# Optimization experiments

Hardware: AMD Instinct MI355X
Metric: run time of the kernel (lower is better)

Reference implementation:

```python
import jax, jax.numpy as jnp
import numpy as np

N = 50000      # nodes
E = 800000     # edges (avg degree 16)
DIN = 128      # input_dim
H = 256        # hidden_channels
DOUT = 64      # output_dim


def _glorot(k, shape):
    lim = float(np.sqrt(6.0 / (shape[0] + shape[1])))
    return jax.random.uniform(k, shape, jnp.float32, -lim, lim)


def setup_inputs() -> dict:
    key = jax.random.key(0)
    ks = jax.random.split(key, 10)
    return {
        "x": jax.random.normal(ks[0], (N, DIN), jnp.float32),
        "W1": _glorot(ks[3], (DIN, H)), "b1": jnp.zeros((H,), jnp.float32),
        "W2": _glorot(ks[4], (H, H)),   "b2": jnp.zeros((H,), jnp.float32),
        "L1w": _glorot(ks[5], (H, DIN)), "L1b": jnp.zeros((DIN,), jnp.float32),
        "L2w": _glorot(ks[6], (DIN, H)), "L2b": jnp.zeros((H,), jnp.float32),
        "W3": _glorot(ks[7], (H, DOUT)), "b3": jnp.zeros((DOUT,), jnp.float32),
        "adj": jax.random.randint(ks[1], (2, E), 0, N),
        "adj2": jax.random.randint(ks[2], (2, E), 0, N),
        "mode": 1,  # 1 -> 'l' (return logits); 0 -> softmax over classes
    }


def gcn_conv(x, edge_index, W, b):
    """PyG-style GCNConv: add self-loops, symmetric D^-1/2 A D^-1/2 norm,
    aggregate neighbor features, then (here fused) linear transform."""
    n = x.shape[0]
    loop = jnp.arange(n)
    src = jnp.concatenate([edge_index[0], loop])  # message sources (j)
    dst = jnp.concatenate([edge_index[1], loop])  # aggregation targets (i)
    deg = jax.ops.segment_sum(jnp.ones(src.shape[0], x.dtype), dst, num_segments=n)
    dinv = jax.lax.rsqrt(jnp.maximum(deg, 1.0))   # deg >= 1 due to self-loops
    norm = dinv[src] * dinv[dst]                  # [E+N]
    h = x @ W                                     # transform first (smaller of the two dims either way)
    msg = h[src] * norm[:, None]                  # gather + scale, [E+N, out]
    return jax.ops.segment_sum(msg, dst, num_segments=n) + b


def reference(x, W1, b1, W2, b2, L1w, L1b, L2w, L2b, W3, b3, adj, adj2, mode):
    h = jax.nn.relu(gcn_conv(x, adj, W1, b1))      # GCNConv(in->h) on adj
    h = jax.nn.relu(gcn_conv(h, adj2, W2, b2))     # GCNConv(h->h) on adj2
    h = jax.nn.relu(h @ L1w + L1b)                 # Linear(h->in)
    h = jax.nn.relu(h @ L2w + L2b)                 # Linear(in->h)
    out = gcn_conv(h, adj2, W3, b3)                # GCNConv(h->out) on adj2
    # dropout has p=0 -> identity
    return out if mode == 1 else jax.nn.softmax(out, axis=1)
```

## Files before the change

### kernel.cpp

```cpp
#include <hip/hip_runtime.h>
#include <hip/hip_bf16.h>
#include <cstdint>
#include <cstddef>

#define NNODES 50000
#define NEDGES 800000
#define D_IN   128
#define D_H    256
#define D_OUT  64
#define BSH    9
#define BKN    (1 << BSH)
#define NBKT   ((NNODES + BKN - 1) / BKN)
#define MAXB   12288
#define CHUNK  2048
#define QMAX   32639.0f

typedef __attribute__((ext_vector_type(8))) short bf16x8;
typedef __attribute__((ext_vector_type(4))) float f32x4;
typedef __attribute__((ext_vector_type(4))) int   i32x4;

__device__ __forceinline__ unsigned short f2bf(float f) {
    unsigned u = __builtin_bit_cast(unsigned, f);
    unsigned r = (u + 0x7FFFu + ((u >> 16) & 1u)) >> 16;
    return (unsigned short)r;
}
__device__ __forceinline__ float bf2f(unsigned short h) {
    unsigned u = ((unsigned)h) << 16;
    return __builtin_bit_cast(float, u);
}


__global__ __launch_bounds__(256) void k_bin(const int* __restrict__ adjA, const int* __restrict__ adjB,
                                             int* __restrict__ bcnt, unsigned* __restrict__ binned, int e) {
    __shared__ int h[NBKT], pfx[NBKT], put[NBKT], gbase[NBKT];
    __shared__ unsigned stage[CHUNK];
    const int g = blockIdx.y;
    const int* srcp = g ? adjB : adjA;
    const int* dstp = srcp + e;
    unsigned* outp = binned + (size_t)g * NBKT * MAXB;
    int* bc = bcnt + g * NBKT;
    const int tid = threadIdx.x;
    const int base = blockIdx.x * CHUNK;
    const int nrem = min(CHUNK, e - base);
    if (nrem <= 0) return;

    for (int t = tid; t < NBKT; t += 256) { h[t] = 0; put[t] = 0; }
    __syncthreads();

    unsigned pv[8];
    int bv[8];
    #pragma unroll
    for (int q = 0; q < 8; ++q) {
        int i = base + q * 256 + tid;
        bv[q] = -1;
        if (i < e) {
            int s = srcp[i];
            int d = dstp[i];
            pv[q] = ((unsigned)d << 16) | (unsigned)s;
            bv[q] = d >> BSH;
            atomicAdd(&h[bv[q]], 1);
        }
    }
    __syncthreads();
    if (tid == 0) {
        int r = 0;
        for (int k = 0; k < NBKT; ++k) { pfx[k] = r; r += h[k]; }
    }
    __syncthreads();
    #pragma unroll
    for (int q = 0; q < 8; ++q) {
        if (bv[q] >= 0) {
            int p = pfx[bv[q]] + atomicAdd(&put[bv[q]], 1);
            stage[p] = pv[q];
        }
    }
    __syncthreads();
    if (tid < NBKT && h[tid] > 0) gbase[tid] = atomicAdd(&bc[tid], h[tid]);
    __syncthreads();
    for (int idx = tid; idx < nrem; idx += 256) {
        unsigned v = stage[idx];
        int bb = v >> (16 + BSH);
        outp[(size_t)bb * MAXB + gbase[bb] + (idx - pfx[bb])] = v;
    }
}

__global__ void k_bktscan(const int* __restrict__ bcnt, int* __restrict__ bbase,
                          int* __restrict__ rp1, int* __restrict__ rp2) {
    __shared__ int s[2][NBKT];
    int t = threadIdx.x;
    if (t < NBKT) s[0][t] = bcnt[t];
    else if (t < 2 * NBKT) s[1][t - NBKT] = bcnt[t];
    __syncthreads();
    if (t < 2) {
        int r = 0;
        for (int k = 0; k < NBKT; ++k) { int v = s[t][k]; s[t][k] = r; r += v; }
    }
    __syncthreads();
    if (t < NBKT) bbase[t] = s[0][t];
    else if (t < 2 * NBKT) bbase[t] = s[1][t - NBKT];
    if (t == 0) { rp1[NNODES] = NEDGES; rp2[NNODES] = NEDGES; }
}

__global__ __launch_bounds__(256) void k_csr_bucket(const unsigned* __restrict__ binned,
                                                    const int* __restrict__ bcnt, const int* __restrict__ bbase,
                                                    int* __restrict__ rp1, int* __restrict__ rp2,
                                                    float* __restrict__ dinv1, float* __restrict__ dinv2,
                                                    int* __restrict__ col1, int* __restrict__ col2, int n) {
    __shared__ int lc[BKN];
    __shared__ int loff[BKN];
    __shared__ int ps[256];
    __shared__ int srt[MAXB];
    const int g = blockIdx.y;
    const int b = blockIdx.x;
    const unsigned* in = binned + (size_t)g * NBKT * MAXB + (size_t)b * MAXB;
    int* rp = g ? rp2 : rp1;
    float* dinv = g ? dinv2 : dinv1;
    int* col = g ? col2 : col1;
    const int nb = bcnt[g * NBKT + b];
    const int base0 = bbase[g * NBKT + b];
    const int nodebase = b << BSH;
    const int tid = threadIdx.x;

    for (int t = tid; t < BKN; t += 256) lc[t] = 0;
    __syncthreads();
    for (int t = tid; t < nb; t += 256)
        atomicAdd(&lc[(in[t] >> 16) & (BKN - 1)], 1);
    __syncthreads();
    int c0 = lc[2 * tid], c1 = lc[2 * tid + 1];
    int pair = c0 + c1;
    int sum = pair;
    ps[tid] = pair;
    __syncthreads();
    #pragma unroll
    for (int off = 1; off < 256; off <<= 1) {
        int u = (tid >= off) ? ps[tid - off] : 0;
        __syncthreads();
        sum += u;
        ps[tid] = sum;
        __syncthreads();
    }
    int excl = sum - pair;
    loff[2 * tid] = excl;
    loff[2 * tid + 1] = excl + c0;
    __syncthreads();
    for (int t = tid; t < BKN; t += 256) {
        int node = nodebase + t;
        if (node < n) {
            rp[node] = base0 + loff[t];
            dinv[node] = rsqrtf((float)(lc[t] + 1));
        }
    }
    __syncthreads();
    for (int t = tid; t < nb; t += 256) {
        unsigned v = in[t];
        int pos = atomicAdd(&loff[(v >> 16) & (BKN - 1)], 1);
        srt[pos] = (int)(v & 0xFFFFu);
    }
    __syncthreads();
    for (int t = tid; t < nb; t += 256) col[base0 + t] = srt[t];
}


template<int F, bool PRESCALE>
__global__ __launch_bounds__(256) void k_quant(const float* __restrict__ in, const float* __restrict__ dscale,
                                               short* __restrict__ q, float* __restrict__ qs, int n) {
    constexpr int VPT = F / 64;
    const int lane = threadIdx.x & 63;
    const int i = blockIdx.x * 4 + (threadIdx.x >> 6);
    if (i >= n) return;
    float v[VPT];
    const float* p = in + (size_t)i * F + lane * VPT;
    if constexpr (VPT == 4) { float4 t = *(const float4*)p; v[0] = t.x; v[1] = t.y; v[2] = t.z; v[3] = t.w; }
    else if constexpr (VPT == 2) { float2 t = *(const float2*)p; v[0] = t.x; v[1] = t.y; }
    else v[0] = *p;
    if constexpr (PRESCALE) {
        float d = dscale[i];
        #pragma unroll
        for (int c = 0; c < VPT; ++c) v[c] *= d;
    }
    float m = 0.f;
    #pragma unroll
    for (int c = 0; c < VPT; ++c) m = fmaxf(m, fabsf(v[c]));
    #pragma unroll
    for (int off = 32; off > 0; off >>= 1) m = fmaxf(m, __shfl_xor(m, off));
    float inv = (m > 0.f) ? 32767.0f / m : 0.f;
    short* qp = q + (size_t)i * F + lane * VPT;
    if constexpr (VPT == 4) {
        short4 o;
        o.x = (short)__float2int_rn(v[0] * inv);
        o.y = (short)__float2int_rn(v[1] * inv);
        o.z = (short)__float2int_rn(v[2] * inv);
        o.w = (short)__float2int_rn(v[3] * inv);
        *(short4*)qp = o;
    } else if constexpr (VPT == 2) {
        short2 o;
        o.x = (short)__float2int_rn(v[0] * inv);
        o.y = (short)__float2int_rn(v[1] * inv);
        *(short2*)qp = o;
    } else {
        *qp = (short)__float2int_rn(v[0] * inv);
    }
    if (lane == 0) qs[i] = m * (1.0f / 32767.0f);
}


template<int F, int OUTM>
__global__ __launch_bounds__(256) void k_agg3(const short* __restrict__ q, const float* __restrict__ qs,
                                              const int* __restrict__ rp, const int* __restrict__ col,
                                              const float* __restrict__ dinv, const float* __restrict__ bias,
                                              void* __restrict__ outv, float* __restrict__ qs_out, int n) {
    constexpr int VPT = F / 64;
    const int lane = threadIdx.x & 63;
    const int i = blockIdx.x * 4 + (threadIdx.x >> 6);
    if (i >= n) return;
    const short* ql = q + lane * VPT;
    float acc[VPT];
    #pragma unroll
    for (int c = 0; c < VPT; ++c) acc[c] = 0.f;

    int k = rp[i], end = rp[i + 1];

    auto body1 = [&](int j) {
        float s = qs[j];
        const short* pj = ql + (size_t)j * F;
        if constexpr (VPT == 4) {
            short4 v = *(const short4*)pj;
            acc[0] += s * (float)v.x; acc[1] += s * (float)v.y;
            acc[2] += s * (float)v.z; acc[3] += s * (float)v.w;
        } else if constexpr (VPT == 2) {
            short2 v = *(const short2*)pj;
            acc[0] += s * (float)v.x; acc[1] += s * (float)v.y;
        } else {
            acc[0] += s * (float)(*pj);
        }
    };

    body1(i);
    if constexpr (VPT == 4) {
        for (; k + 8 <= end; k += 8) {
            int j[8]; float s[8]; short4 v[8];
            #pragma unroll
            for (int u = 0; u < 8; ++u) j[u] = col[k + u];
            #pragma unroll
            for (int u = 0; u < 8; ++u) s[u] = qs[j[u]];
            #pragma unroll
            for (int u = 0; u < 8; ++u) v[u] = *(const short4*)(ql + (size_t)j[u] * F);
            #pragma unroll
            for (int u = 0; u < 8; ++u) {
                acc[0] += s[u] * (float)v[u].x; acc[1] += s[u] * (float)v[u].y;
                acc[2] += s[u] * (float)v[u].z; acc[3] += s[u] * (float)v[u].w;
            }
        }
    } else if constexpr (VPT == 2) {
        for (; k + 8 <= end; k += 8) {
            int j[8]; float s[8]; short2 v[8];
            #pragma unroll
            for (int u = 0; u < 8; ++u) j[u] = col[k + u];
            #pragma unroll
            for (int u = 0; u < 8; ++u) s[u] = qs[j[u]];
            #pragma unroll
            for (int u = 0; u < 8; ++u) v[u] = *(const short2*)(ql + (size_t)j[u] * F);
            #pragma unroll
            for (int u = 0; u < 8; ++u) {
                acc[0] += s[u] * (float)v[u].x; acc[1] += s[u] * (float)v[u].y;
            }
        }
    }
    for (; k + 4 <= end; k += 4) {
        int j0 = col[k], j1 = col[k + 1], j2 = col[k + 2], j3 = col[k + 3];
        float s0 = qs[j0], s1 = qs[j1], s2 = qs[j2], s3 = qs[j3];
        if constexpr (VPT == 4) {
            short4 v0 = *(const short4*)(ql + (size_t)j0 * F);
            short4 v1 = *(const short4*)(ql + (size_t)j1 * F);
            short4 v2 = *(const short4*)(ql + (size_t)j2 * F);
            short4 v3 = *(const short4*)(ql + (size_t)j3 * F);
            acc[0] += s0 * (float)v0.x + s1 * (float)v1.x + s2 * (float)v2.x + s3 * (float)v3.x;
            acc[1] += s0 * (float)v0.y + s1 * (float)v1.y + s2 * (float)v2.y + s3 * (float)v3.y;
            acc[2] += s0 * (float)v0.z + s1 * (float)v1.z + s2 * (float)v2.z + s3 * (float)v3.z;
            acc[3] += s0 * (float)v0.w + s1 * (float)v1.w + s2 * (float)v2.w + s3 * (float)v3.w;
        } else if constexpr (VPT == 2) {
            short2 v0 = *(const short2*)(ql + (size_t)j0 * F);
            short2 v1 = *(const short2*)(ql + (size_t)j1 * F);
            short2 v2 = *(const short2*)(ql + (size_t)j2 * F);
            short2 v3 = *(const short2*)(ql + (size_t)j3 * F);
            acc[0] += s0 * (float)v0.x + s1 * (float)v1.x + s2 * (float)v2.x + s3 * (float)v3.x;
            acc[1] += s0 * (float)v0.y + s1 * (float)v1.y + s2 * (float)v2.y + s3 * (float)v3.y;
        } else {
            float v0 = (float)ql[(size_t)j0 * F];
            float v1 = (float)ql[(size_t)j1 * F];
            float v2 = (float)ql[(size_t)j2 * F];
            float v3 = (float)ql[(size_t)j3 * F];
            acc[0] += s0 * v0 + s1 * v1 + s2 * v2 + s3 * v3;
        }
    }
    for (; k < end; ++k) body1(col[k]);

    float di = dinv[i];
    if constexpr (OUTM == 0) {
        float vals[VPT];
        float m = 0.f;
        #pragma unroll
        for (int c = 0; c < VPT; ++c) { vals[c] = acc[c] * di; m = fmaxf(m, fabsf(vals[c])); }
        #pragma unroll
        for (int off = 32; off > 0; off >>= 1) m = fmaxf(m, __shfl_xor(m, off));
        float inv = (m > 0.f) ? QMAX / m : 0.f;
        unsigned ph = 0, pl = 0;
        #pragma unroll
        for (int c = 0; c < VPT; ++c) {
            int qv = __float2int_rn(vals[c] * inv);
            int ah = (qv + 128) >> 8;
            int al = qv - (ah << 8);
            ph |= (unsigned)(ah & 0xFF) << (8 * c);
            pl |= (unsigned)(al & 0xFF) << (8 * c);
        }
        unsigned char* o8h = (unsigned char*)outv;
        unsigned char* o8l = o8h + (size_t)n * F;
        if constexpr (VPT == 4) {
            *(unsigned*)(o8h + (size_t)i * F + lane * 4) = ph;
            *(unsigned*)(o8l + (size_t)i * F + lane * 4) = pl;
        } else if constexpr (VPT == 2) {
            *(unsigned short*)(o8h + (size_t)i * F + lane * 2) = (unsigned short)ph;
            *(unsigned short*)(o8l + (size_t)i * F + lane * 2) = (unsigned short)pl;
        } else {
            o8h[(size_t)i * F + lane] = (unsigned char)ph;
            o8l[(size_t)i * F + lane] = (unsigned char)pl;
        }
        if (lane == 0) qs_out[i] = m * (1.0f / QMAX);
    } else {
        float* o = (float*)outv + (size_t)i * F + lane * VPT;
        #pragma unroll
        for (int c = 0; c < VPT; ++c) o[c] = acc[c] * di + bias[lane * VPT + c];
    }
}


__device__ __forceinline__ void wconv1(const float* __restrict__ W, unsigned short* __restrict__ Th,
                                       unsigned short* __restrict__ Tl, int idx, int K, int Nc) {
    int k = idx / Nc, n = idx - k * Nc;
    float v = W[idx];
    unsigned short h = f2bf(v);
    unsigned short l = f2bf(v - bf2f(h));
    Th[(size_t)n * K + k] = h;
    Tl[(size_t)n * K + k] = l;
}

__global__ void k_wconv_all(const float* L1w, const float* L2w, const float* W3,
                            unsigned short* L1h, unsigned short* L1l, unsigned short* L2h, unsigned short* L2l,
                            unsigned short* W3h, unsigned short* W3l) {
    int idx = blockIdx.x * blockDim.x + threadIdx.x;
    if (idx < 32768)        wconv1(L1w, L1h, L1l, idx, D_H, D_IN);
    else if (idx < 65536)   wconv1(L2w, L2h, L2l, idx - 32768, D_IN, D_H);
    else if (idx < 81920)   wconv1(W3, W3h, W3l, idx - 65536, D_H, D_OUT);
}


__global__ __launch_bounds__(256) void k_wconv_i8(const float* __restrict__ W1, const float* __restrict__ W2,
        signed char* __restrict__ B1h, signed char* __restrict__ B1l,
        signed char* __restrict__ B2h, signed char* __restrict__ B2l,
        float* __restrict__ ws1, float* __restrict__ ws2) {
    const int c4 = blockIdx.x * 4 + (threadIdx.x >> 6);
    const int lane = threadIdx.x & 63;
    const float* W; signed char *Bh, *Bl; float* ws; int K, c;
    if (c4 < 256) { W = W1; Bh = B1h; Bl = B1l; ws = ws1; K = D_IN; c = c4; }
    else          { W = W2; Bh = B2h; Bl = B2l; ws = ws2; K = D_H;  c = c4 - 256; }
    float m = 0.f;
    for (int k = lane; k < K; k += 64) m = fmaxf(m, fabsf(W[(size_t)k * D_H + c]));
    #pragma unroll
    for (int off = 32; off > 0; off >>= 1) m = fmaxf(m, __shfl_xor(m, off));
    float inv = (m > 0.f) ? QMAX / m : 0.f;
    for (int k = lane; k < K; k += 64) {
        int qv = __float2int_rn(W[(size_t)k * D_H + c] * inv);
        int ah = (qv + 128) >> 8;
        int al = qv - (ah << 8);
        Bh[(size_t)c * K + k] = (signed char)ah;
        Bl[(size_t)c * K + k] = (signed char)al;
    }
    if (lane == 0) ws[c] = m * (1.0f / QMAX);
}


template<bool RELU, bool BIAS, int OUTM>
__global__ __launch_bounds__(256) void k_gemm_i8(const unsigned char* __restrict__ A8,
        const float* __restrict__ qsr,
        const signed char* __restrict__ B8h, const signed char* __restrict__ B8l,
        const float* __restrict__ wsc,
        const float* __restrict__ bias, const float* __restrict__ dscale,
        void* __restrict__ Cv, int M, int K, int Nc, int ncb) {
    constexpr int PADB = 68;
    __shared__ unsigned char As_h[128][PADB];
    __shared__ unsigned char As_l[128][PADB];
    __shared__ unsigned char Bs_h[64][PADB];
    __shared__ unsigned char Bs_l[64][PADB];

    const int nwg = gridDim.x;
    const int b = blockIdx.x;
    const int q8 = nwg >> 3, r8 = nwg & 7;
    const int xcd = b & 7;
    const int swz = (xcd < r8 ? xcd * (q8 + 1) : r8 * (q8 + 1) + (xcd - r8) * q8) + (b >> 3);
    const int row0 = (swz / ncb) * 128;
    const int col0 = (swz % ncb) * 64;

    const int tid = threadIdx.x;
    const int lane = tid & 63;
    const int wv = tid >> 6;

    i32x4 acc_hh[2][4], acc_mm[2][4];
    #pragma unroll
    for (int m = 0; m < 2; ++m)
        #pragma unroll
        for (int n = 0; n < 4; ++n) {
            acc_hh[m][n] = (i32x4)(0);
            acc_mm[m][n] = (i32x4)(0);
        }

    const int srow = tid >> 1;
    const int skh = (tid & 1) * 32;
    int arow = row0 + srow;
    if (arow >= M) arow = M - 1;
    const unsigned char* aph = A8 + (size_t)arow * K + skh;
    const unsigned char* apl = aph + (size_t)M * K;

    const int bn = tid >> 2;
    const int bko = (tid & 3) * 16;
    const signed char* bph = B8h + (size_t)(col0 + bn) * K + bko;
    const signed char* bpl = B8l + (size_t)(col0 + bn) * K + bko;

    const int fr = lane & 15;
    const int fko = (lane >> 4) * 16;

    const int nk = K >> 6;
    for (int kt = 0; kt < nk; ++kt) {
        uint4 ah0 = *(const uint4*)(aph + kt * 64);
        uint4 ah1 = *(const uint4*)(aph + kt * 64 + 16);
        uint4 al0 = *(const uint4*)(apl + kt * 64);
        uint4 al1 = *(const uint4*)(apl + kt * 64 + 16);
        uint4 bh0 = *(const uint4*)(bph + kt * 64);
        uint4 bl0 = *(const uint4*)(bpl + kt * 64);

        __syncthreads();

        *(uint4*)&As_h[srow][skh] = ah0;
        *(uint4*)&As_h[srow][skh + 16] = ah1;
        *(uint4*)&As_l[srow][skh] = al0;
        *(uint4*)&As_l[srow][skh + 16] = al1;
        *(uint4*)&Bs_h[bn][bko] = bh0;
        *(uint4*)&Bs_l[bn][bko] = bl0;

        __syncthreads();

        i32x4 fah[2], fal[2], fbh[4], fbl[4];
        #pragma unroll
        for (int m = 0; m < 2; ++m) {
            fah[m] = *(const i32x4*)&As_h[wv * 32 + m * 16 + fr][fko];
            fal[m] = *(const i32x4*)&As_l[wv * 32 + m * 16 + fr][fko];
        }
        #pragma unroll
        for (int n = 0; n < 4; ++n) {
            fbh[n] = *(const i32x4*)&Bs_h[n * 16 + fr][fko];
            fbl[n] = *(const i32x4*)&Bs_l[n * 16 + fr][fko];
        }
        #pragma unroll
        for (int m = 0; m < 2; ++m)
            #pragma unroll
            for (int n = 0; n < 4; ++n) {
                acc_hh[m][n] = __builtin_amdgcn_mfma_i32_16x16x64_i8(fah[m], fbh[n], acc_hh[m][n], 0, 0, 0);
                acc_mm[m][n] = __builtin_amdgcn_mfma_i32_16x16x64_i8(fah[m], fbl[n], acc_mm[m][n], 0, 0, 0);
                acc_mm[m][n] = __builtin_amdgcn_mfma_i32_16x16x64_i8(fal[m], fbh[n], acc_mm[m][n], 0, 0, 0);
            }
    }

    float bv[4], wv_[4];
    #pragma unroll
    for (int n = 0; n < 4; ++n) {
        const int c = col0 + n * 16 + fr;
        bv[n] = BIAS ? bias[c] : 0.f;
        wv_[n] = wsc[c];
    }
    const int rbase = row0 + wv * 32 + (lane >> 4) * 4;
    #pragma unroll
    for (int m = 0; m < 2; ++m) {
        #pragma unroll
        for (int j = 0; j < 4; ++j) {
            const int r = rbase + m * 16 + j;
            if (r >= M) continue;
            const float qr = qsr[r];
            float ds = 1.f;
            if constexpr (OUTM == 1) ds = dscale[r];
            #pragma unroll
            for (int n = 0; n < 4; ++n) {
                const int c = col0 + n * 16 + fr;
                float dot = 65536.f * (float)acc_hh[m][n][j] + 256.f * (float)acc_mm[m][n][j];
                float o = dot * qr * wv_[n] + bv[n];
                if constexpr (RELU) o = fmaxf(o, 0.f);
                if constexpr (OUTM == 1) {
                    ((float*)Cv)[(size_t)r * Nc + c] = o * ds;
                } else {
                    unsigned short h = f2bf(o);
                    unsigned short l = f2bf(o - bf2f(h));
                    unsigned short* C2 = (unsigned short*)Cv + (size_t)r * 2 * Nc + c;
                    C2[0] = h;
                    C2[Nc] = l;
                }
            }
        }
    }
}


template<bool RELU, bool BIAS, int OUTM>
__global__ __launch_bounds__(256) void k_gemm3(const unsigned short* __restrict__ Ahl,
        const unsigned short* __restrict__ Bth, const unsigned short* __restrict__ Btl,
        const float* __restrict__ bias, const float* __restrict__ dscale,
        void* __restrict__ Cv, float* __restrict__ qs_out, int M, int K, int Nc, int ncb) {
    constexpr int PAD = 66;
    __shared__ unsigned short As_h[128][PAD];
    __shared__ unsigned short As_l[128][PAD];
    __shared__ unsigned short Bs_h[64][PAD];
    __shared__ unsigned short Bs_l[64][PAD];

    const int nwg = gridDim.x;
    const int b = blockIdx.x;
    const int q8 = nwg >> 3, r8 = nwg & 7;
    const int xcd = b & 7;
    const int swz = (xcd < r8 ? xcd * (q8 + 1) : r8 * (q8 + 1) + (xcd - r8) * q8) + (b >> 3);
    const int row0 = (swz / ncb) * 128;
    const int col0 = (swz % ncb) * 64;

    const int tid = threadIdx.x;
    const int lane = tid & 63;
    const int wv = tid >> 6;

    f32x4 acc[2][4];
    #pragma unroll
    for (int m = 0; m < 2; ++m)
        #pragma unroll
        for (int n = 0; n < 4; ++n) acc[m][n] = (f32x4)(0.f);

    const int srow = tid >> 1;
    const int skh = (tid & 1) * 32;
    int arow = row0 + srow;
    if (arow >= M) arow = M - 1;
    const unsigned short* aph = Ahl + (size_t)arow * 2 * K + skh;
    const unsigned short* apl = aph + K;

    const int bn = tid >> 2;
    const int bko = (tid & 3) * 16;
    const unsigned short* bph = Bth + (size_t)(col0 + bn) * K + bko;
    const unsigned short* bpl = Btl + (size_t)(col0 + bn) * K + bko;

    const int fr = lane & 15;
    const int fk = (lane >> 4) * 8;

    const int nk = K >> 6;
    for (int kt = 0; kt < nk; ++kt) {
        uint4 ah0 = *(const uint4*)(aph + kt * 64);
        uint4 ah1 = *(const uint4*)(aph + kt * 64 + 8);
        uint4 ah2 = *(const uint4*)(aph + kt * 64 + 16);
        uint4 ah3 = *(const uint4*)(aph + kt * 64 + 24);
        uint4 al0 = *(const uint4*)(apl + kt * 64);
        uint4 al1 = *(const uint4*)(apl + kt * 64 + 8);
        uint4 al2 = *(const uint4*)(apl + kt * 64 + 16);
        uint4 al3 = *(const uint4*)(apl + kt * 64 + 24);
        uint4 bh0 = *(const uint4*)(bph + kt * 64);
        uint4 bh1 = *(const uint4*)(bph + kt * 64 + 8);
        uint4 bl0 = *(const uint4*)(bpl + kt * 64);
        uint4 bl1 = *(const uint4*)(bpl + kt * 64 + 8);

        __syncthreads();

        *(uint4*)&As_h[srow][skh] = ah0;
        *(uint4*)&As_h[srow][skh + 8] = ah1;
        *(uint4*)&As_h[srow][skh + 16] = ah2;
        *(uint4*)&As_h[srow][skh + 24] = ah3;
        *(uint4*)&As_l[srow][skh] = al0;
        *(uint4*)&As_l[srow][skh + 8] = al1;
        *(uint4*)&As_l[srow][skh + 16] = al2;
        *(uint4*)&As_l[srow][skh + 24] = al3;
        *(uint4*)&Bs_h[bn][bko] = bh0;
        *(uint4*)&Bs_h[bn][bko + 8] = bh1;
        *(uint4*)&Bs_l[bn][bko] = bl0;
        *(uint4*)&Bs_l[bn][bko + 8] = bl1;

        __syncthreads();

        #pragma unroll
        for (int ks = 0; ks < 2; ++ks) {
            const int ko = ks * 32 + fk;
            bf16x8 ah[2], al[2], bh[4], bl[4];
            #pragma unroll
            for (int m = 0; m < 2; ++m) {
                ah[m] = *(const bf16x8*)&As_h[wv * 32 + m * 16 + fr][ko];
                al[m] = *(const bf16x8*)&As_l[wv * 32 + m * 16 + fr][ko];
            }
            #pragma unroll
            for (int n = 0; n < 4; ++n) {
                bh[n] = *(const bf16x8*)&Bs_h[n * 16 + fr][ko];
                bl[n] = *(const bf16x8*)&Bs_l[n * 16 + fr][ko];
            }
            #pragma unroll
            for (int m = 0; m < 2; ++m)
                #pragma unroll
                for (int n = 0; n < 4; ++n) {
                    acc[m][n] = __builtin_amdgcn_mfma_f32_16x16x32_bf16(ah[m], bh[n], acc[m][n], 0, 0, 0);
                    acc[m][n] = __builtin_amdgcn_mfma_f32_16x16x32_bf16(ah[m], bl[n], acc[m][n], 0, 0, 0);
                    acc[m][n] = __builtin_amdgcn_mfma_f32_16x16x32_bf16(al[m], bh[n], acc[m][n], 0, 0, 0);
                }
        }
    }

    const int rbase = row0 + wv * 32 + (lane >> 4) * 4;
    if constexpr (OUTM == 3) {
        #pragma unroll
        for (int m = 0; m < 2; ++m) {
            #pragma unroll
            for (int j = 0; j < 4; ++j) {
                const int r = rbase + m * 16 + j;
                const int rr = (r < M) ? r : (M - 1);
                const float ds = dscale[rr];
                float vals[4];
                float mx = 0.f;
                #pragma unroll
                for (int n = 0; n < 4; ++n) {
                    float o = acc[m][n][j] * ds;
                    vals[n] = o;
                    mx = fmaxf(mx, fabsf(o));
                }
                mx = fmaxf(mx, __shfl_xor(mx, 1));
                mx = fmaxf(mx, __shfl_xor(mx, 2));
                mx = fmaxf(mx, __shfl_xor(mx, 4));
                mx = fmaxf(mx, __shfl_xor(mx, 8));
                float inv = (mx > 0.f) ? 32767.0f / mx : 0.f;
                if (r < M) {
                    short* C2 = (short*)Cv + (size_t)r * Nc;
                    #pragma unroll
                    for (int n = 0; n < 4; ++n)
                        C2[n * 16 + fr] = (short)__float2int_rn(vals[n] * inv);
                    if (fr == 0) qs_out[r] = mx * (1.0f / 32767.0f);
                }
            }
        }
        return;
    }

    float bv[4];
    #pragma unroll
    for (int n = 0; n < 4; ++n) bv[n] = BIAS ? bias[col0 + n * 16 + fr] : 0.f;
    #pragma unroll
    for (int m = 0; m < 2; ++m) {
        #pragma unroll
        for (int j = 0; j < 4; ++j) {
            const int r = rbase + m * 16 + j;
            if (r >= M) continue;
            float ds = 1.f;
            if constexpr (OUTM == 1) ds = dscale[r];
            #pragma unroll
            for (int n = 0; n < 4; ++n) {
                const int c = col0 + n * 16 + fr;
                float o = acc[m][n][j] + bv[n];
                if constexpr (RELU) o = fmaxf(o, 0.f);
                if constexpr (OUTM == 1) {
                    ((float*)Cv)[(size_t)r * Nc + c] = o * ds;
                } else {
                    unsigned short h = f2bf(o);
                    unsigned short l = f2bf(o - bf2f(h));
                    unsigned short* C2 = (unsigned short*)Cv + (size_t)r * 2 * Nc + c;
                    C2[0] = h;
                    C2[Nc] = l;
                }
            }
        }
    }
}


__global__ __launch_bounds__(256) void k_softmax(float* __restrict__ out, const int* __restrict__ mode, int n) {
    if (*mode == 1) return;
    int lane = threadIdx.x & 63;
    int i = blockIdx.x * 4 + (threadIdx.x >> 6);
    if (i >= n) return;
    float v = out[(size_t)i * 64 + lane];
    float m = v;
    #pragma unroll
    for (int off = 32; off > 0; off >>= 1) m = fmaxf(m, __shfl_xor(m, off));
    float e = __expf(v - m);
    float s = e;
    #pragma unroll
    for (int off = 32; off > 0; off >>= 1) s += __shfl_xor(s, off);
    out[(size_t)i * 64 + lane] = e / s;
}


extern "C" void kernel_launch(void* const* d_in, const int* in_sizes, int n_in,
                              void* d_out, int out_size, void* d_ws, size_t ws_size,
                              hipStream_t stream) {
    const float* x   = (const float*)d_in[0];
    const float* W1  = (const float*)d_in[1];
    const float* b1  = (const float*)d_in[2];
    const float* W2  = (const float*)d_in[3];
    const float* b2  = (const float*)d_in[4];
    const float* L1w = (const float*)d_in[5];
    const float* L1b = (const float*)d_in[6];
    const float* L2w = (const float*)d_in[7];
    const float* L2b = (const float*)d_in[8];
    const float* W3  = (const float*)d_in[9];
    const float* b3  = (const float*)d_in[10];
    const int* adj   = (const int*)d_in[11];
    const int* adj2  = (const int*)d_in[12];
    const int* mode  = (const int*)d_in[13];
    float* out = (float*)d_out;

    char* ws = (char*)d_ws;
    auto alloc = [&](size_t bytes) {
        char* p = ws;
        ws += (bytes + 255) & ~(size_t)255;
        return p;
    };
    char*  bufA  = alloc((size_t)NNODES * 256 * 4);
    char*  bufB  = alloc((size_t)NNODES * 256 * 4);
    int*   rp1   = (int*)alloc((NNODES + 1) * 4);
    int*   col1  = (int*)alloc((size_t)NEDGES * 4);
    int*   rp2   = (int*)alloc((NNODES + 1) * 4);
    int*   col2  = (int*)alloc((size_t)NEDGES * 4);
    float* dinv1 = (float*)alloc(NNODES * 4);
    float* dinv2 = (float*)alloc(NNODES * 4);
    int*   bcnt  = (int*)alloc(2 * NBKT * 4);
    int*   bbase = (int*)alloc(2 * NBKT * 4);
    float* qsA   = (float*)alloc(NNODES * 4);
    float* qsB   = (float*)alloc(NNODES * 4);
    signed char* B1h = (signed char*)alloc(256 * D_IN);
    signed char* B1l = (signed char*)alloc(256 * D_IN);
    signed char* B2h = (signed char*)alloc(256 * D_H);
    signed char* B2l = (signed char*)alloc(256 * D_H);
    float* ws1 = (float*)alloc(256 * 4);
    float* ws2 = (float*)alloc(256 * 4);
    unsigned short* L1h = (unsigned short*)alloc(D_H * D_IN * 2);
    unsigned short* L1l = (unsigned short*)alloc(D_H * D_IN * 2);
    unsigned short* L2h = (unsigned short*)alloc(D_IN * D_H * 2);
    unsigned short* L2l = (unsigned short*)alloc(D_IN * D_H * 2);
    unsigned short* W3h = (unsigned short*)alloc(D_H * D_OUT * 2);
    unsigned short* W3l = (unsigned short*)alloc(D_H * D_OUT * 2);
    unsigned* binned = (unsigned*)bufA;

    const int AGB = (NNODES + 3) / 4;
    const int MT = (NNODES + 127) / 128;
    const int BINB = (NEDGES + CHUNK - 1) / CHUNK;

    k_wconv_all<<<(81920 + 255) / 256, 256, 0, stream>>>(L1w, L2w, W3,
        L1h, L1l, L2h, L2l, W3h, W3l);
    k_wconv_i8<<<128, 256, 0, stream>>>(W1, W2, B1h, B1l, B2h, B2l, ws1, ws2);

    hipMemsetAsync(bcnt, 0, 2 * NBKT * 4, stream);
    k_bin<<<dim3(BINB, 2), 256, 0, stream>>>(adj, adj2, bcnt, binned, NEDGES);
    k_bktscan<<<1, 256, 0, stream>>>(bcnt, bbase, rp1, rp2);
    k_csr_bucket<<<dim3(NBKT, 2), 256, 0, stream>>>(binned, bcnt, bbase, rp1, rp2,
                                                    dinv1, dinv2, col1, col2, NNODES);

    k_quant<128, true><<<AGB, 256, 0, stream>>>(x, dinv1, (short*)bufA, qsA, NNODES);
    k_agg3<128, 0><<<AGB, 256, 0, stream>>>((const short*)bufA, qsA, rp1, col1, dinv1, nullptr, bufB, qsB, NNODES);
    k_gemm_i8<true, true, 1><<<MT * 4, 256, 0, stream>>>(
        (const unsigned char*)bufB, qsB, B1h, B1l, ws1, b1, dinv2, bufA, NNODES, D_IN, D_H, 4);
    k_quant<256, false><<<AGB, 256, 0, stream>>>((const float*)bufA, nullptr, (short*)bufB, qsA, NNODES);
    k_agg3<256, 0><<<AGB, 256, 0, stream>>>((const short*)bufB, qsA, rp2, col2, dinv2, nullptr, bufA, qsB, NNODES);
    k_gemm_i8<true, true, 2><<<MT * 4, 256, 0, stream>>>(
        (const unsigned char*)bufA, qsB, B2h, B2l, ws2, b2, nullptr, bufB, NNODES, D_H, D_H, 4);
    k_gemm3<true, true, 2><<<MT * 2, 256, 0, stream>>>(
        (const unsigned short*)bufB, L1h, L1l, L1b, nullptr, bufA, nullptr, NNODES, D_H, D_IN, 2);
    k_gemm3<true, true, 2><<<MT * 4, 256, 0, stream>>>(
        (const unsigned short*)bufA, L2h, L2l, L2b, nullptr, bufB, nullptr, NNODES, D_IN, D_H, 4);
    k_gemm3<false, false, 3><<<MT * 1, 256, 0, stream>>>(
        (const unsigned short*)bufB, W3h, W3l, nullptr, dinv2, bufA, qsA, NNODES, D_H, D_OUT, 1);
    k_agg3<64, 1><<<AGB, 256, 0, stream>>>((const short*)bufA, qsA, rp2, col2, dinv2, b3, out, nullptr, NNODES);
    k_softmax<<<AGB, 256, 0, stream>>>(out, mode, NNODES);
}
```

Before: 326.3 us.

## Fuse int16 quantization into first int8 GEMM epilogue with per-block scales

The first int8 GEMM now quantizes its output directly to int16 inside the epilogue. Each row gets one scale per 64-column block, found with a shuffle max-reduction across the 16 lanes, instead of a float32 row being written and then re-quantized by a separate kernel. The second aggregation kernel reads these per-block scales through a new QSB template parameter. This removes one full float32 write and read of a 50000x256 activation and one kernel launch. The cost is extra shuffle work in the GEMM epilogue and an extra scale gather per edge in the aggregation.

```diff
diff --git a/kernel.cpp b/kernel.cpp
--- a/kernel.cpp
+++ b/kernel.cpp
@@ -204,7 +204,7 @@
 }
 
 
-template<int F, int OUTM>
+template<int F, int OUTM, int QSB>
 __global__ __launch_bounds__(256) void k_agg3(const short* __restrict__ q, const float* __restrict__ qs,
                                               const int* __restrict__ rp, const int* __restrict__ col,
                                               const float* __restrict__ dinv, const float* __restrict__ bias,
@@ -213,6 +213,7 @@
     const int lane = threadIdx.x & 63;
     const int i = blockIdx.x * 4 + (threadIdx.x >> 6);
     if (i >= n) return;
+    const int cb = (QSB == 1) ? 0 : ((lane * VPT) >> 6);
     const short* ql = q + lane * VPT;
     float acc[VPT];
     #pragma unroll
@@ -221,7 +222,7 @@
     int k = rp[i], end = rp[i + 1];
 
     auto body1 = [&](int j) {
-        float s = qs[j];
+        float s = qs[j * QSB + cb];
         const short* pj = ql + (size_t)j * F;
         if constexpr (VPT == 4) {
             short4 v = *(const short4*)pj;
@@ -242,7 +243,7 @@
             #pragma unroll
             for (int u = 0; u < 8; ++u) j[u] = col[k + u];
             #pragma unroll
-            for (int u = 0; u < 8; ++u) s[u] = qs[j[u]];
+            for (int u = 0; u < 8; ++u) s[u] = qs[j[u] * QSB + cb];
             #pragma unroll
             for (int u = 0; u < 8; ++u) v[u] = *(const short4*)(ql + (size_t)j[u] * F);
             #pragma unroll
@@ -257,7 +258,7 @@
             #pragma unroll
             for (int u = 0; u < 8; ++u) j[u] = col[k + u];
             #pragma unroll
-            for (int u = 0; u < 8; ++u) s[u] = qs[j[u]];
+            for (int u = 0; u < 8; ++u) s[u] = qs[j[u] * QSB + cb];
             #pragma unroll
             for (int u = 0; u < 8; ++u) v[u] = *(const short2*)(ql + (size_t)j[u] * F);
             #pragma unroll
@@ -268,7 +269,8 @@
     }
     for (; k + 4 <= end; k += 4) {
         int j0 = col[k], j1 = col[k + 1], j2 = col[k + 2], j3 = col[k + 3];
-        float s0 = qs[j0], s1 = qs[j1], s2 = qs[j2], s3 = qs[j3];
+        float s0 = qs[j0 * QSB + cb], s1 = qs[j1 * QSB + cb];
+        float s2 = qs[j2 * QSB + cb], s3 = qs[j3 * QSB + cb];
         if constexpr (VPT == 4) {
             short4 v0 = *(const short4*)(ql + (size_t)j0 * F);
             short4 v1 = *(const short4*)(ql + (size_t)j1 * F);
@@ -385,7 +387,7 @@
         const signed char* __restrict__ B8h, const signed char* __restrict__ B8l,
         const float* __restrict__ wsc,
         const float* __restrict__ bias, const float* __restrict__ dscale,
-        void* __restrict__ Cv, int M, int K, int Nc, int ncb) {
+        void* __restrict__ Cv, float* __restrict__ qs_out, int M, int K, int Nc, int ncb) {
     constexpr int PADB = 68;
     __shared__ unsigned char As_h[128][PADB];
     __shared__ unsigned char As_l[128][PADB];
@@ -477,6 +479,44 @@
         wv_[n] = wsc[c];
     }
     const int rbase = row0 + wv * 32 + (lane >> 4) * 4;
+
+    if constexpr (OUTM == 4) {
+        #pragma unroll
+        for (int m = 0; m < 2; ++m) {
+            #pragma unroll
+            for (int j = 0; j < 4; ++j) {
+                const int r = rbase + m * 16 + j;
+                const int rr = (r < M) ? r : (M - 1);
+                const float qr = qsr[rr];
+                const float ds = dscale[rr];
+                float vals[4];
+                float mx = 0.f;
+                #pragma unroll
+                for (int n = 0; n < 4; ++n) {
+                    float dot = 65536.f * (float)acc_hh[m][n][j] + 256.f * (float)acc_mm[m][n][j];
+                    float o = dot * qr * wv_[n] + bv[n];
+                    if constexpr (RELU) o = fmaxf(o, 0.f);
+                    o *= ds;
+                    vals[n] = o;
+                    mx = fmaxf(mx, fabsf(o));
+                }
+                mx = fmaxf(mx, __shfl_xor(mx, 1));
+                mx = fmaxf(mx, __shfl_xor(mx, 2));
+                mx = fmaxf(mx, __shfl_xor(mx, 4));
+                mx = fmaxf(mx, __shfl_xor(mx, 8));
+                float inv = (mx > 0.f) ? 32767.0f / mx : 0.f;
+                if (r < M) {
+                    short* C2 = (short*)Cv + (size_t)r * Nc + col0;
+                    #pragma unroll
+                    for (int n = 0; n < 4; ++n)
+                        C2[n * 16 + fr] = (short)__float2int_rn(vals[n] * inv);
+                    if (fr == 0) qs_out[(size_t)r * ncb + (col0 >> 6)] = mx * (1.0f / 32767.0f);
+                }
+            }
+        }
+        return;
+    }
+
     #pragma unroll
     for (int m = 0; m < 2; ++m) {
         #pragma unroll
@@ -727,6 +767,7 @@
     int*   bbase = (int*)alloc(2 * NBKT * 4);
     float* qsA   = (float*)alloc(NNODES * 4);
     float* qsB   = (float*)alloc(NNODES * 4);
+    float* qsA4  = (float*)alloc((size_t)NNODES * 4 * 4);
     signed char* B1h = (signed char*)alloc(256 * D_IN);
     signed char* B1l = (signed char*)alloc(256 * D_IN);
     signed char* B2h = (signed char*)alloc(256 * D_H);
@@ -756,19 +797,18 @@
                                                     dinv1, dinv2, col1, col2, NNODES);
 
     k_quant<128, true><<<AGB, 256, 0, stream>>>(x, dinv1, (short*)bufA, qsA, NNODES);
-    k_agg3<128, 0><<<AGB, 256, 0, stream>>>((const short*)bufA, qsA, rp1, col1, dinv1, nullptr, bufB, qsB, NNODES);
-    k_gemm_i8<true, true, 1><<<MT * 4, 256, 0, stream>>>(
-        (const unsigned char*)bufB, qsB, B1h, B1l, ws1, b1, dinv2, bufA, NNODES, D_IN, D_H, 4);
-    k_quant<256, false><<<AGB, 256, 0, stream>>>((const float*)bufA, nullptr, (short*)bufB, qsA, NNODES);
-    k_agg3<256, 0><<<AGB, 256, 0, stream>>>((const short*)bufB, qsA, rp2, col2, dinv2, nullptr, bufA, qsB, NNODES);
+    k_agg3<128, 0, 1><<<AGB, 256, 0, stream>>>((const short*)bufA, qsA, rp1, col1, dinv1, nullptr, bufB, qsB, NNODES);
+    k_gemm_i8<true, true, 4><<<MT * 4, 256, 0, stream>>>(
+        (const unsigned char*)bufB, qsB, B1h, B1l, ws1, b1, dinv2, bufA, qsA4, NNODES, D_IN, D_H, 4);
+    k_agg3<256, 0, 4><<<AGB, 256, 0, stream>>>((const short*)bufA, qsA4, rp2, col2, dinv2, nullptr, bufB, qsB, NNODES);
     k_gemm_i8<true, true, 2><<<MT * 4, 256, 0, stream>>>(
-        (const unsigned char*)bufA, qsB, B2h, B2l, ws2, b2, nullptr, bufB, NNODES, D_H, D_H, 4);
+        (const unsigned char*)bufB, qsB, B2h, B2l, ws2, b2, nullptr, bufA, nullptr, NNODES, D_H, D_H, 4);
     k_gemm3<true, true, 2><<<MT * 2, 256, 0, stream>>>(
-        (const unsigned short*)bufB, L1h, L1l, L1b, nullptr, bufA, nullptr, NNODES, D_H, D_IN, 2);
+        (const unsigned short*)bufA, L1h, L1l, L1b, nullptr, bufB, nullptr, NNODES, D_H, D_IN, 2);
     k_gemm3<true, true, 2><<<MT * 4, 256, 0, stream>>>(
-        (const unsigned short*)bufA, L2h, L2l, L2b, nullptr, bufB, nullptr, NNODES, D_IN, D_H, 4);
+        (const unsigned short*)bufB, L2h, L2l, L2b, nullptr, bufA, nullptr, NNODES, D_IN, D_H, 4);
     k_gemm3<false, false, 3><<<MT * 1, 256, 0, stream>>>(
-        (const unsigned short*)bufB, W3h, W3l, nullptr, dinv2, bufA, qsA, NNODES, D_H, D_OUT, 1);
-    k_agg3<64, 1><<<AGB, 256, 0, stream>>>((const short*)bufA, qsA, rp2, col2, dinv2, b3, out, nullptr, NNODES);
+        (const unsigned short*)bufA, W3h, W3l, nullptr, dinv2, bufB, qsA, NNODES, D_H, D_OUT, 1);
+    k_agg3<64, 1, 1><<<AGB, 256, 0, stream>>>((const short*)bufB, qsA, rp2, col2, dinv2, b3, out, nullptr, NNODES);
     k_softmax<<<AGB, 256, 0, stream>>>(out, mode, NNODES);
 }
```

Measured after the change: 324.0 us. Within noise of the previous version (-0.7%).
